# Kernel tuning notes

Measured on AMD Instinct MI355X. Metric: run time of the kernel, lower is better.

Reference implementation:

```python
import jax, jax.numpy as jnp
import numpy as np

N = 8000      # nodes
E = 64000     # edges
F = 2560      # in_channels
H = 8         # heads
C = 320       # out_channels per head
G = 16        # graphs in batch
SLOPE = 0.2   # GATv2 default negative_slope


def setup_inputs() -> dict:
    key = jax.random.key(0)
    ks = jax.random.split(key, 20)
    inp = {
        'x': jax.random.normal(ks[0], (N, F), jnp.float32),
        'edge_index': jax.random.randint(ks[1], (2, E), 0, N, dtype=jnp.int64),
        'edge_attr': jax.random.normal(ks[2], (E, 1), jnp.float32),
        'batch': jnp.sort(jax.random.randint(ks[3], (N,), 0, G, dtype=jnp.int64)),
    }
    s_in = 1.0 / np.sqrt(F).astype(np.float32)
    s_att = 1.0 / np.sqrt(C).astype(np.float32)
    k = 4
    for layer in (1, 2):
        inp[f'Wl{layer}'] = jax.random.normal(ks[k + 0], (F, H * C), jnp.float32) * s_in
        inp[f'bl{layer}'] = jnp.zeros((H * C,), jnp.float32)
        inp[f'Wr{layer}'] = jax.random.normal(ks[k + 1], (F, H * C), jnp.float32) * s_in
        inp[f'br{layer}'] = jnp.zeros((H * C,), jnp.float32)
        inp[f'We{layer}'] = jax.random.normal(ks[k + 2], (1, H * C), jnp.float32)
        inp[f'att{layer}'] = jax.random.normal(ks[k + 3], (H, C), jnp.float32) * s_att
        inp[f'bias{layer}'] = jnp.zeros((H * C,), jnp.float32)
        k += 4
    return inp


def gatv2_layer(x, src, dst, edge_attr, Wl, bl, Wr, br, We, att, bias):
    # x: [N,F] -> out: [N, H*C]
    xl = (x @ Wl + bl).reshape(N, H, C)   # source transform (aggregated)
    xr = (x @ Wr + br).reshape(N, H, C)   # target transform
    ee = (edge_attr @ We).reshape(E, H, C)
    m = jax.nn.leaky_relu(xl[src] + xr[dst] + ee, SLOPE)  # [E,H,C]
    score = jnp.einsum('ehc,hc->eh', m, att)               # [E,H]
    # segment softmax over incoming edges of each target node
    smax = jax.ops.segment_max(score, dst, num_segments=N)  # [N,H]
    ex = jnp.exp(score - smax[dst])
    denom = jax.ops.segment_sum(ex, dst, num_segments=N)    # [N,H]
    alpha = ex / denom[dst]                                  # [E,H]
    out = jax.ops.segment_sum(xl[src] * alpha[:, :, None], dst, num_segments=N)
    return out.reshape(N, H * C) + bias


def reference(x, edge_index, edge_attr, batch,
              Wl1, bl1, Wr1, br1, We1, att1, bias1,
              Wl2, bl2, Wr2, br2, We2, att2, bias2):
    src, dst = edge_index[0], edge_index[1]
    h = gatv2_layer(x, src, dst, edge_attr, Wl1, bl1, Wr1, br1, We1, att1, bias1)
    # dropout is identity in eval mode
    h = gatv2_layer(h, src, dst, edge_attr, Wl2, bl2, Wr2, br2, We2, att2, bias2)
    # global mean pool over graphs
    sums = jax.ops.segment_sum(h, batch, num_segments=G)                 # [G, H*C]
    cnt = jax.ops.segment_sum(jnp.ones((N, 1), h.dtype), batch, num_segments=G)
    return sums / jnp.maximum(cnt, 1.0)
```

## Files before the change

kernel.cpp:

```cpp
#include <hip/hip_runtime.h>

typedef unsigned short u16;
typedef _Float16 f16;
typedef _Float16 f16x8 __attribute__((ext_vector_type(8)));
typedef _Float16 f16x2 __attribute__((ext_vector_type(2)));
typedef float f32x4 __attribute__((ext_vector_type(4)));

#define AS1 __attribute__((address_space(1)))
#define AS3 __attribute__((address_space(3)))

constexpr int N_NODES = 8000;
constexpr int N_EDGES = 64000;
constexpr int F_IN    = 2560;
constexpr int HEADS   = 8;
constexpr int CPH     = 320;
constexpr int HC      = 2560;
constexpr int NW      = 5120;
constexpr int NGRAPH  = 16;
constexpr float SLOPE = 0.2f;

__global__ __launch_bounds__(256)
void cvt_f32_f16(const float* __restrict__ in, f16* __restrict__ out, int n)
{
  const int i = (blockIdx.x * 256 + threadIdx.x) * 4;
  if (i >= n) return;
  const float4 v = *(const float4*)(in + i);
  f16 o[4] = {(f16)v.x, (f16)v.y, (f16)v.z, (f16)v.w};
  *(ushort4*)(out + i) = *(const ushort4*)o;
}

__global__ __launch_bounds__(256)
void transpose_w(const float* __restrict__ in, f16* __restrict__ out)
{
  __shared__ u16 tile[64][66];
  const int bx = blockIdx.x * 64;
  const int by = blockIdx.y * 64;
  const int tx = threadIdx.x & 63;
  const int ty = threadIdx.x >> 6;
  #pragma unroll
  for (int i = ty; i < 64; i += 4) {
    f16 h = (f16)in[(size_t)(by + i) * HC + bx + tx];
    u16 u; __builtin_memcpy(&u, &h, 2);
    tile[i][tx] = u;
  }
  __syncthreads();
  #pragma unroll
  for (int i = ty; i < 64; i += 4) {
    u16 u = tile[tx][i];
    f16 h; __builtin_memcpy(&h, &u, 2);
    out[(size_t)(bx + i) * F_IN + by + tx] = h;
  }
}

__global__ __launch_bounds__(512, 2)
void gemm_fused(const f16* __restrict__ A, const f16* __restrict__ BT,
                const float* __restrict__ bl, const float* __restrict__ br,
                f16* __restrict__ XL, f16* __restrict__ XR)
{
  __shared__ __align__(16) f16 sm[65536];
  f16* const sA0 = sm;
  f16* const sA1 = sm + 16384;
  f16* const sB0 = sm + 32768;
  f16* const sB1 = sm + 49152;

  const int t    = threadIdx.x;
  const int lane = t & 63;
  const int wave = t >> 6;

  const int bid0 = (int)blockIdx.x;
  const int xcd  = bid0 & 7;
  const int ic   = bid0 >> 3;
  const int m0   = (xcd * 4 + (ic & 3)) * 256;
  const int n0   = (ic >> 2) * 256;

  const int fm = (wave >> 2) * 128;
  const int fn = (wave & 3) * 64;
  const int ml = lane & 15;
  const int lq = lane >> 4;

  auto stageA = [&](f16* D, int half, int kt) {
    const int k0 = kt * 64;
    #pragma unroll
    for (int jj = 0; jj < 2; ++jj) {
      const int s  = jj * 512 + t;
      const int r  = s >> 3;
      const int lc = (s & 7) ^ (r & 7);
      int gr = m0 + half * 128 + r;
      gr = (gr < N_NODES) ? gr : (N_NODES - 1);
      const f16* g = A + (size_t)gr * F_IN + k0 + lc * 8;
      __builtin_amdgcn_global_load_lds((AS1 const void*)g,
                                       (AS3 void*)(D + half * 8192 + s * 8), 16, 0, 0);
    }
  };
  auto stageB = [&](f16* D, int half, int kt) {
    const int k0 = kt * 64;
    #pragma unroll
    for (int jj = 0; jj < 2; ++jj) {
      const int s  = jj * 512 + t;
      const int r  = s >> 3;
      const int lc = (s & 7) ^ (r & 7);
      const f16* g = BT + (size_t)(n0 + half * 128 + r) * F_IN + k0 + lc * 8;
      __builtin_amdgcn_global_load_lds((AS1 const void*)g,
                                       (AS3 void*)(D + half * 8192 + s * 8), 16, 0, 0);
    }
  };
  auto ldA = [&](const f16* S, int i, int kk) -> f16x8 {
    const int row = fm + i * 16 + ml;
    const int p   = (kk * 4 + lq) ^ (row & 7);
    return *(const f16x8*)(S + row * 64 + p * 8);
  };
  auto ldB = [&](const f16* S, int j, int kk) -> f16x8 {
    const int row = fn + j * 16 + ml;
    const int p   = (kk * 4 + lq) ^ (row & 7);
    return *(const f16x8*)(S + row * 64 + p * 8);
  };

  f32x4 acc[8][4] = {};
  f16x8 bf[4][2];

#define MMROW(i, A0_, A1_)                                                                   \
    _Pragma("unroll")                                                                        \
    for (int j = 0; j < 4; ++j) {                                                            \
      acc[i][j] = __builtin_amdgcn_mfma_f32_16x16x32_f16(A0_, bf[j][0], acc[i][j], 0, 0, 0); \
      acc[i][j] = __builtin_amdgcn_mfma_f32_16x16x32_f16(A1_, bf[j][1], acc[i][j], 0, 0, 0); \
    }

#define PHASE(SA, q, STG)                          \
  {                                                \
    STG;                                           \
    const f16x8 p00 = ldA(SA, 2*(q),     0);       \
    const f16x8 p01 = ldA(SA, 2*(q),     1);       \
    const f16x8 p10 = ldA(SA, 2*(q) + 1, 0);       \
    const f16x8 p11 = ldA(SA, 2*(q) + 1, 1);       \
    __builtin_amdgcn_s_barrier();                  \
    __builtin_amdgcn_s_setprio(1);                 \
    MMROW(2*(q),     p00, p01)                     \
    MMROW(2*(q) + 1, p10, p11)                     \
    __builtin_amdgcn_s_setprio(0);                 \
  }

#define ENDPH() { __builtin_amdgcn_s_barrier(); }
#define LOADB(SB) { _Pragma("unroll") for (int j = 0; j < 4; ++j) { bf[j][0] = ldB(SB, j, 0); bf[j][1] = ldB(SB, j, 1); } }

  stageA(sA0, 0, 0); stageA(sA0, 1, 0);
  stageB(sB0, 0, 0); stageB(sB0, 1, 0);
  stageB(sB1, 0, 1); stageB(sB1, 1, 1);
  asm volatile("s_waitcnt vmcnt(4)" ::: "memory");
  __builtin_amdgcn_s_barrier();

  for (int it = 0; it < 20; ++it) {
    const int T  = 2 * it;
    const int t1 = T + 1;
    const int t2 = (T + 2 < 40) ? T + 2 : 39;
    const int t3 = (T + 3 < 40) ? T + 3 : 39;

    LOADB(sB0)
    PHASE(sA0, 0, stageA(sA1, 0, t1)) ENDPH()
    PHASE(sA0, 1, stageA(sA1, 1, t1)) ENDPH()
    PHASE(sA0, 2, stageB(sB0, 0, t2)) ENDPH()
    PHASE(sA0, 3, stageB(sB0, 1, t2))
    asm volatile("s_waitcnt vmcnt(4)" ::: "memory");
    ENDPH()
    LOADB(sB1)
    PHASE(sA1, 0, stageA(sA0, 0, t2)) ENDPH()
    PHASE(sA1, 1, stageA(sA0, 1, t2)) ENDPH()
    PHASE(sA1, 2, stageB(sB1, 0, t3)) ENDPH()
    PHASE(sA1, 3, stageB(sB1, 1, t3))
    asm volatile("s_waitcnt vmcnt(4)" ::: "memory");
    ENDPH()
  }

#undef MMROW
#undef PHASE
#undef ENDPH
#undef LOADB

  asm volatile("s_waitcnt vmcnt(0)" ::: "memory");
  __builtin_amdgcn_s_barrier();

  const bool left = (n0 < HC);
  f16* __restrict__ OUT = left ? XL : XR;
  const float* __restrict__ bias = left ? bl : br;
  const int nb = left ? n0 : (n0 - HC);
  const int rg = (lane >> 4) * 4;
  f16* const wbase = sm + wave * 8192;

  #pragma unroll
  for (int j = 0; j < 4; ++j) {
    const float bv = bias[nb + fn + j * 16 + ml];
    #pragma unroll
    for (int i = 0; i < 8; ++i) {
      #pragma unroll
      for (int r = 0; r < 4; ++r) {
        const int row = i * 16 + rg + r;
        const int col = j * 16 + ml;
        const int pc  = (col >> 3) ^ (row & 7);
        wbase[row * 64 + pc * 8 + (col & 7)] = (f16)(acc[i][j][r] + bv);
      }
    }
  }
  __syncthreads();
  #pragma unroll
  for (int it = 0; it < 16; ++it) {
    const int row = it * 8 + (lane >> 3);
    const int ch  = lane & 7;
    const int pc  = ch ^ (row & 7);
    const f16x8 v = *(const f16x8*)(wbase + row * 64 + pc * 8);
    const int gm = m0 + fm + row;
    if (gm < N_NODES)
      *(f16x8*)(OUT + (size_t)gm * HC + nb + fn + ch * 8) = v;
  }
}

__global__ __launch_bounds__(256)
void count_edges(const int* __restrict__ dst, int* __restrict__ counts)
{
  const int e = blockIdx.x * 256 + threadIdx.x;
  if (e < N_EDGES) atomicAdd(&counts[dst[e]], 1);
}

__global__ __launch_bounds__(256)
void scan_offsets(const int* __restrict__ counts, int* __restrict__ offs, int* __restrict__ cur)
{
  __shared__ int wtot[4];
  const int t = threadIdx.x;
  const int lane = t & 63, wave = t >> 6;
  const int base = t * 32;
  int loc[32];
  int run = 0;
  #pragma unroll
  for (int i = 0; i < 32; ++i) {
    const int idx = base + i;
    const int v = (idx < N_NODES) ? counts[idx] : 0;
    loc[i] = run;
    run += v;
  }
  int incl = run;
  #pragma unroll
  for (int off = 1; off < 64; off <<= 1) {
    int y = __shfl_up(incl, off, 64);
    if (lane >= off) incl += y;
  }
  const int excl = incl - run;
  if (lane == 63) wtot[wave] = incl;
  __syncthreads();
  int wb = 0;
  for (int wv = 0; wv < wave; ++wv) wb += wtot[wv];
  const int mybase = wb + excl;
  #pragma unroll
  for (int i = 0; i < 32; ++i) {
    const int idx = base + i;
    if (idx < N_NODES) { offs[idx] = mybase + loc[i]; cur[idx] = mybase + loc[i]; }
  }
  if (t == 255) offs[N_NODES] = wb + incl;
}

__global__ __launch_bounds__(256)
void fill_csr(const int* __restrict__ dst, const int* __restrict__ srcv,
              const float* __restrict__ ea, int* __restrict__ cur,
              int2* __restrict__ ecsr)
{
  const int e = blockIdx.x * 256 + threadIdx.x;
  if (e < N_EDGES) {
    const int p = atomicAdd(&cur[dst[e]], 1);
    ecsr[p] = make_int2(srcv[e], __float_as_int(ea[e]));
  }
}

__global__ __launch_bounds__(256)
void gat_edge_fused(const f16* __restrict__ XL, const f16* __restrict__ XR,
                    const float* __restrict__ We, const float* __restrict__ att,
                    const int2* __restrict__ ecsr, const int* __restrict__ offs,
                    const float* __restrict__ bias,
                    f16* __restrict__ out)
{
  const int n    = blockIdx.x;
  const int t    = threadIdx.x;
  const int wave = t >> 6;
  const int lane = t & 63;
  const int half = lane >> 5;
  const int l32  = lane & 31;
  const int h    = wave * 2 + half;
  const int c8   = h * CPH + l32 * 8;
  const int c2   = h * CPH + 256 + l32 * 2;

  float xr[10], wv[10], av[10];
  {
    const f16x8 v8 = *(const f16x8*)(XR + (size_t)n * HC + c8);
    const f16x2 v2 = *(const f16x2*)(XR + (size_t)n * HC + c2);
    #pragma unroll
    for (int k = 0; k < 8; ++k) xr[k] = (float)v8[k];
    xr[8] = (float)v2[0]; xr[9] = (float)v2[1];
  }
  {
    const float4 w0 = *(const float4*)(We + c8);
    const float4 w1 = *(const float4*)(We + c8 + 4);
    const float4 a0 = *(const float4*)(att + c8);
    const float4 a1 = *(const float4*)(att + c8 + 4);
    wv[0]=w0.x; wv[1]=w0.y; wv[2]=w0.z; wv[3]=w0.w;
    wv[4]=w1.x; wv[5]=w1.y; wv[6]=w1.z; wv[7]=w1.w;
    av[0]=a0.x; av[1]=a0.y; av[2]=a0.z; av[3]=a0.w;
    av[4]=a1.x; av[5]=a1.y; av[6]=a1.z; av[7]=a1.w;
    wv[8] = We[c2]; wv[9] = We[c2 + 1];
    av[8] = att[c2]; av[9] = att[c2 + 1];
  }

  float m = -3.0e38f, l = 0.f;
  float acc[10];
  #pragma unroll
  for (int k = 0; k < 10; ++k) acc[k] = 0.f;

  const int b = offs[n], e = offs[n + 1];
  if (b < e) {
    int2 mA = ecsr[b];
    f16x8 v8A = *(const f16x8*)(XL + (size_t)mA.x * HC + c8);
    f16x2 v2A = *(const f16x2*)(XL + (size_t)mA.x * HC + c2);
    int2 mB = (b + 1 < e) ? ecsr[b + 1] : make_int2(mA.x, 0);

    for (int p = b; p < e; ++p) {
      const f16* rowN = XL + (size_t)mB.x * HC;
      const f16x8 v8N = *(const f16x8*)(rowN + c8);
      const f16x2 v2N = *(const f16x2*)(rowN + c2);
      const int pn = (p + 2 < e) ? (p + 2) : (e - 1);
      const int2 mC = ecsr[pn];

      const float ea = __int_as_float(mA.y);
      float xl[10];
      #pragma unroll
      for (int k = 0; k < 8; ++k) xl[k] = (float)v8A[k];
      xl[8] = (float)v2A[0]; xl[9] = (float)v2A[1];
      float partial = 0.f;
      #pragma unroll
      for (int k = 0; k < 10; ++k) {
        float v = xl[k] + xr[k] + ea * wv[k];
        v = (v > 0.f) ? v : SLOPE * v;
        partial += v * av[k];
      }
      #pragma unroll
      for (int msk = 16; msk >= 1; msk >>= 1)
        partial += __shfl_xor(partial, msk, 64);
      const float sc    = partial;
      const float mn    = fmaxf(m, sc);
      const float scale = __expf(m - mn);
      const float w     = __expf(sc - mn);
      l = l * scale + w;
      #pragma unroll
      for (int k = 0; k < 10; ++k) acc[k] = acc[k] * scale + w * xl[k];
      m = mn;

      mA = mB; v8A = v8N; v2A = v2N; mB = mC;
    }
  }

  const float inv = (l > 0.f) ? 1.f / l : 0.f;
  f16x8 s8;
  #pragma unroll
  for (int k = 0; k < 8; ++k) s8[k] = (f16)(acc[k] * inv + bias[c8 + k]);
  f16x2 s2;
  s2[0] = (f16)(acc[8] * inv + bias[c2]);
  s2[1] = (f16)(acc[9] * inv + bias[c2 + 1]);
  *(f16x8*)(out + (size_t)n * HC + c8) = s8;
  *(f16x2*)(out + (size_t)n * HC + c2) = s2;
}

__global__ __launch_bounds__(256)
void pool_kernel(const f16* __restrict__ Hm, const int* __restrict__ batch, float* __restrict__ out)
{
  __shared__ int se[2];
  const int g = blockIdx.x;
  const int chunk = blockIdx.y;
  const int t = threadIdx.x;
  if (t < 2) {
    const int target = g + t;
    int lo = 0, hi = N_NODES;
    while (lo < hi) { const int mid = (lo + hi) >> 1; if (batch[mid] < target) lo = mid + 1; else hi = mid; }
    se[t] = lo;
  }
  __syncthreads();
  const int s0 = se[0], s1 = se[1];
  const int c = chunk * 256 + t;
  float sum = 0.f;
  for (int n = s0; n < s1; ++n) sum += (float)Hm[(size_t)n * HC + c];
  int cnt = s1 - s0; if (cnt < 1) cnt = 1;
  out[g * HC + c] = sum / (float)cnt;
}

static void run_layer(const f16* A, const float* Wl, const float* bl,
                      const float* Wr, const float* br,
                      const float* We, const float* att, const float* bias,
                      f16* WT, f16* XL, f16* XR,
                      const int* offs, const int2* ecsr, f16* OUT, hipStream_t stream)
{
  dim3 tgrid(HC / 64, F_IN / 64);
  transpose_w<<<tgrid, 256, 0, stream>>>(Wl, WT);
  transpose_w<<<tgrid, 256, 0, stream>>>(Wr, WT + (size_t)HC * F_IN);
  gemm_fused<<<32 * (NW / 256), 512, 0, stream>>>(A, WT, bl, br, XL, XR);
  gat_edge_fused<<<N_NODES, 256, 0, stream>>>(XL, XR, We, att, ecsr, offs, bias, OUT);
}

extern "C" void kernel_launch(void* const* d_in, const int* in_sizes, int n_in,
                              void* d_out, int out_size, void* d_ws, size_t ws_size,
                              hipStream_t stream)
{
  const float* x     = (const float*)d_in[0];
  const int*   eidx  = (const int*)d_in[1];
  const float* eattr = (const float*)d_in[2];
  const int*   batch = (const int*)d_in[3];
  const float* Wl1  = (const float*)d_in[4];
  const float* bl1  = (const float*)d_in[5];
  const float* Wr1  = (const float*)d_in[6];
  const float* br1  = (const float*)d_in[7];
  const float* We1  = (const float*)d_in[8];
  const float* att1 = (const float*)d_in[9];
  const float* bias1= (const float*)d_in[10];
  const float* Wl2  = (const float*)d_in[11];
  const float* bl2  = (const float*)d_in[12];
  const float* Wr2  = (const float*)d_in[13];
  const float* br2  = (const float*)d_in[14];
  const float* We2  = (const float*)d_in[15];
  const float* att2 = (const float*)d_in[16];
  const float* bias2= (const float*)d_in[17];
  float* out = (float*)d_out;

  const int* src = eidx;
  const int* dst = eidx + N_EDGES;

  char* w = (char*)d_ws;
  auto take = [&](size_t b) { char* p = w; w += (b + 255) & ~(size_t)255; return p; };
  f16*   Xh    = (f16*)take((size_t)N_NODES * F_IN * 2);
  f16*   H2h   = (f16*)take((size_t)N_NODES * HC * 2);
  f16*   WT    = (f16*)take((size_t)NW * F_IN * 2);
  f16*   XL    = (f16*)take((size_t)N_NODES * HC * 2);
  f16*   XR    = (f16*)take((size_t)N_NODES * HC * 2);
  int*   counts= (int*)take((size_t)N_NODES * 4);
  int*   offs  = (int*)take((size_t)(N_NODES + 1) * 4);
  int*   cur   = (int*)take((size_t)N_NODES * 4);
  int2*  ecsr  = (int2*)take((size_t)N_EDGES * 8);

  hipMemsetAsync(counts, 0, N_NODES * 4, stream);
  count_edges<<<N_EDGES / 256, 256, 0, stream>>>(dst, counts);
  scan_offsets<<<1, 256, 0, stream>>>(counts, offs, cur);
  fill_csr<<<N_EDGES / 256, 256, 0, stream>>>(dst, src, eattr, cur, ecsr);

  cvt_f32_f16<<<(N_NODES * F_IN) / 1024, 256, 0, stream>>>(x, Xh, N_NODES * F_IN);

  run_layer(Xh, Wl1, bl1, Wr1, br1, We1, att1, bias1,
            WT, XL, XR, offs, ecsr, Xh, stream);
  run_layer(Xh, Wl2, bl2, Wr2, br2, We2, att2, bias2,
            WT, XL, XR, offs, ecsr, H2h, stream);

  pool_kernel<<<dim3(NGRAPH, HC / 256), 256, 0, stream>>>(H2h, batch, out);
}
```

Before: 907.1 us.

## Restructure GEMM main loop to single-stage double buffering with one barrier per tile

Replaces the two-tile-per-iteration ping-pong schedule, which had a workgroup barrier after every quarter phase, with a simpler loop over 40 K tiles. Each iteration reads the current buffers and issues global-to-LDS staging for the next tile, then ends with a single vmcnt(0) wait and barrier. The sched_barrier calls keep the compiler from reordering across phases. This removes most of the per-phase barriers, at the cost of a shallower prefetch (one tile ahead instead of two for B) and a full drain of outstanding loads on every iteration.

```diff
diff --git a/kernel.cpp b/kernel.cpp
--- a/kernel.cpp
+++ b/kernel.cpp
@@ -125,58 +125,70 @@
       acc[i][j] = __builtin_amdgcn_mfma_f32_16x16x32_f16(A1_, bf[j][1], acc[i][j], 0, 0, 0); \
     }
 
-#define PHASE(SA, q, STG)                          \
-  {                                                \
-    STG;                                           \
-    const f16x8 p00 = ldA(SA, 2*(q),     0);       \
-    const f16x8 p01 = ldA(SA, 2*(q),     1);       \
-    const f16x8 p10 = ldA(SA, 2*(q) + 1, 0);       \
-    const f16x8 p11 = ldA(SA, 2*(q) + 1, 1);       \
-    __builtin_amdgcn_s_barrier();                  \
-    __builtin_amdgcn_s_setprio(1);                 \
-    MMROW(2*(q),     p00, p01)                     \
-    MMROW(2*(q) + 1, p10, p11)                     \
-    __builtin_amdgcn_s_setprio(0);                 \
-  }
-
-#define ENDPH() { __builtin_amdgcn_s_barrier(); }
+#define SBAR0() __builtin_amdgcn_sched_barrier(0)
 #define LOADB(SB) { _Pragma("unroll") for (int j = 0; j < 4; ++j) { bf[j][0] = ldB(SB, j, 0); bf[j][1] = ldB(SB, j, 1); } }
 
   stageA(sA0, 0, 0); stageA(sA0, 1, 0);
   stageB(sB0, 0, 0); stageB(sB0, 1, 0);
-  stageB(sB1, 0, 1); stageB(sB1, 1, 1);
-  asm volatile("s_waitcnt vmcnt(4)" ::: "memory");
-  __builtin_amdgcn_s_barrier();
-
-  for (int it = 0; it < 20; ++it) {
-    const int T  = 2 * it;
-    const int t1 = T + 1;
-    const int t2 = (T + 2 < 40) ? T + 2 : 39;
-    const int t3 = (T + 3 < 40) ? T + 3 : 39;
-
-    LOADB(sB0)
-    PHASE(sA0, 0, stageA(sA1, 0, t1)) ENDPH()
-    PHASE(sA0, 1, stageA(sA1, 1, t1)) ENDPH()
-    PHASE(sA0, 2, stageB(sB0, 0, t2)) ENDPH()
-    PHASE(sA0, 3, stageB(sB0, 1, t2))
-    asm volatile("s_waitcnt vmcnt(4)" ::: "memory");
-    ENDPH()
-    LOADB(sB1)
-    PHASE(sA1, 0, stageA(sA0, 0, t2)) ENDPH()
-    PHASE(sA1, 1, stageA(sA0, 1, t2)) ENDPH()
-    PHASE(sA1, 2, stageB(sB1, 0, t3)) ENDPH()
-    PHASE(sA1, 3, stageB(sB1, 1, t3))
-    asm volatile("s_waitcnt vmcnt(4)" ::: "memory");
-    ENDPH()
-  }
-
-#undef MMROW
-#undef PHASE
-#undef ENDPH
-#undef LOADB
-
   asm volatile("s_waitcnt vmcnt(0)" ::: "memory");
   __builtin_amdgcn_s_barrier();
+  SBAR0();
+
+  for (int T = 0; T < 40; ++T) {
+    f16* const rA = (T & 1) ? sA1 : sA0;
+    f16* const rB = (T & 1) ? sB1 : sB0;
+    f16* const wA = (T & 1) ? sA0 : sA1;
+    f16* const wB = (T & 1) ? sB0 : sB1;
+    const int Tn = (T + 1 < 40) ? (T + 1) : 39;
+
+    LOADB(rB)
+    {
+      const f16x8 a00 = ldA(rA, 0, 0), a01 = ldA(rA, 0, 1);
+      const f16x8 a10 = ldA(rA, 1, 0), a11 = ldA(rA, 1, 1);
+      stageA(wA, 0, Tn); stageA(wA, 1, Tn);
+      __builtin_amdgcn_s_setprio(1);
+      MMROW(0, a00, a01)
+      MMROW(1, a10, a11)
+      __builtin_amdgcn_s_setprio(0);
+    }
+    SBAR0();
+    {
+      const f16x8 a00 = ldA(rA, 2, 0), a01 = ldA(rA, 2, 1);
+      const f16x8 a10 = ldA(rA, 3, 0), a11 = ldA(rA, 3, 1);
+      stageB(wB, 0, Tn); stageB(wB, 1, Tn);
+      __builtin_amdgcn_s_setprio(1);
+      MMROW(2, a00, a01)
+      MMROW(3, a10, a11)
+      __builtin_amdgcn_s_setprio(0);
+    }
+    SBAR0();
+    {
+      const f16x8 a00 = ldA(rA, 4, 0), a01 = ldA(rA, 4, 1);
+      const f16x8 a10 = ldA(rA, 5, 0), a11 = ldA(rA, 5, 1);
+      __builtin_amdgcn_s_setprio(1);
+      MMROW(4, a00, a01)
+      MMROW(5, a10, a11)
+      __builtin_amdgcn_s_setprio(0);
+    }
+    SBAR0();
+    {
+      const f16x8 a00 = ldA(rA, 6, 0), a01 = ldA(rA, 6, 1);
+      const f16x8 a10 = ldA(rA, 7, 0), a11 = ldA(rA, 7, 1);
+      __builtin_amdgcn_s_setprio(1);
+      MMROW(6, a00, a01)
+      MMROW(7, a10, a11)
+      __builtin_amdgcn_s_setprio(0);
+    }
+    asm volatile("s_waitcnt vmcnt(0)" ::: "memory");
+    __builtin_amdgcn_s_barrier();
+    SBAR0();
+  }
+
+#undef MMROW
+#undef SBAR0
+#undef LOADB
+
+  __syncthreads();
 
   const bool left = (n0 < HC);
   f16* __restrict__ OUT = left ? XL : XR;
```

New measurement: 883.1 us. -2.6%, faster.
